# Performance work log

Measured on AMD Instinct MI355X. Metric: run time of the kernel, lower is better.

## Reference

```python
import jax, jax.numpy as jnp
import numpy as np

D = 1024
M = 256
BATCH = 2048


def setup_inputs() -> dict:
    key = jax.random.key(0)
    kx, kw, kp = jax.random.split(key, 3)
    x = jax.random.uniform(kx, (BATCH, D), dtype=jnp.float32)
    W = jax.random.normal(kw, (M,), dtype=jnp.float32)
    P = jax.random.normal(kp, (M, D), dtype=jnp.float32)
    return {"x": x, "W": W, "P": P}


def reference(x, W, P):
    # log mixture weights: log softmax over m
    logw = jax.nn.log_softmax(W, axis=-1)              # [m]
    p = jax.nn.sigmoid(P)                              # [m, d]
    # broadcast Bernoulli likelihood: [batch, m, d]
    lik = x[:, None, :] * p[None, :, :] + (1.0 - x[:, None, :]) * (1.0 - p[None, :, :])
    # per-component log-likelihood summed over features, plus log weight
    comp_ll = jnp.sum(jnp.log(lik), axis=-1) + logw[None, :]   # [batch, m]
    # mixture log-likelihood via logsumexp over components
    return jax.scipy.special.logsumexp(comp_ll, axis=-1)       # [batch]
```

## Files before the change

### kernel.cpp

```cpp
#include <hip/hip_runtime.h>

#define BATCH 2048
#define MM    256
#define DD    1024

#define BB 128
#define BM 64
#define DC 64
#define SD (DD / DC)
#define NBT (BATCH / BB)
#define XS_TILE (DC * BB)
#define RS_TILE (DC * BM)

#define LOG2E 1.4426950408889634f
#define LN2   0.6931471805599453f

typedef float v2f __attribute__((ext_vector_type(2)));

__device__ __forceinline__ float fr_mant(float x) {
    return __builtin_amdgcn_frexp_mantf(x);
}
__device__ __forceinline__ int fr_exp(float x) {
    return __builtin_amdgcn_frexp_expf(x);
}

__device__ __forceinline__ unsigned short f2bf(float f) {
    unsigned u = __float_as_uint(f);
    u += 0x7FFFu + ((u >> 16) & 1u);
    return (unsigned short)(u >> 16);
}
__device__ __forceinline__ float bf2f(unsigned short u) {
    return __uint_as_float((unsigned)u << 16);
}

__device__ __forceinline__ void gl_lds16(const float* g, float* l) {
    __builtin_amdgcn_global_load_lds(
        (const __attribute__((address_space(1))) unsigned int*)g,
        (__attribute__((address_space(3))) unsigned int*)l, 16, 0, 0);
}

__global__ __launch_bounds__(256) void precomp_kernel(
        const float* __restrict__ P, const float* __restrict__ Wv,
        float* __restrict__ rbuf, float* __restrict__ cst) {
    const int m = blockIdx.x;
    const int t = threadIdx.x;
    const int lane = t & 63, wid = t >> 6;

    float4 z = ((const float4*)(P + (size_t)m * DD))[t];
    float e0 = __expf(z.x), e1 = __expf(z.y), e2 = __expf(z.z), e3 = __expf(z.w);
    ((float4*)(rbuf + (size_t)m * DD))[t] =
        make_float4(e0 - 1.f, e1 - 1.f, e2 - 1.f, e3 - 1.f);
    float part = -(__log2f(1.f + e0) + __log2f(1.f + e1) +
                   __log2f(1.f + e2) + __log2f(1.f + e3));

    __shared__ float smA[4], smB[4];

    #pragma unroll
    for (int o = 32; o; o >>= 1) part += __shfl_xor(part, o);
    if (lane == 0) smA[wid] = part;

    float w = Wv[t];
    float mx = w;
    #pragma unroll
    for (int o = 32; o; o >>= 1) mx = fmaxf(mx, __shfl_xor(mx, o));
    if (lane == 0) smB[wid] = mx;
    __syncthreads();

    float rowc = smA[0] + smA[1] + smA[2] + smA[3];
    float gmx  = fmaxf(fmaxf(smB[0], smB[1]), fmaxf(smB[2], smB[3]));

    float se = __expf(w - gmx);
    #pragma unroll
    for (int o = 32; o; o >>= 1) se += __shfl_xor(se, o);
    __syncthreads();
    if (lane == 0) smA[wid] = se;
    __syncthreads();

    if (t == 0) {
        float sum = smA[0] + smA[1] + smA[2] + smA[3];
        cst[m] = rowc + (Wv[m] - gmx) * LOG2E - __log2f(sum);
    }
}

__global__ __launch_bounds__(256) void swz_kernel(
        const float* __restrict__ x, const float* __restrict__ rbuf,
        float* __restrict__ xs, float* __restrict__ rs) {
    __shared__ float t[128 * 65];
    const int tid = threadIdx.x;
    const int bx = blockIdx.x, by = blockIdx.y;

    const float* src;
    float* dst;
    int rows;
    if (bx < NBT) {
        rows = BB;
        src = x + (size_t)bx * BB * DD + by * DC;
        dst = xs + ((size_t)bx * SD + by) * XS_TILE;
    } else {
        rows = BM;
        src = rbuf + (size_t)(bx - NBT) * BM * DD + by * DC;
        dst = rs + ((size_t)(bx - NBT) * SD + by) * RS_TILE;
    }

    const int nf4 = rows * (DC / 4);
    for (int k = 0; k < nf4 / 256; ++k) {
        int idx4 = tid + 256 * k;
        int row = idx4 >> 4;
        int c4  = idx4 & 15;
        float4 v = *(const float4*)(src + (size_t)row * DD + c4 * 4);
        t[row * 65 + c4 * 4 + 0] = v.x;
        t[row * 65 + c4 * 4 + 1] = v.y;
        t[row * 65 + c4 * 4 + 2] = v.z;
        t[row * 65 + c4 * 4 + 3] = v.w;
    }
    __syncthreads();
    const int r4 = rows >> 2;
    for (int k = 0; k < nf4 / 256; ++k) {
        int o4 = tid + 256 * k;
        int kc  = o4 / r4;
        int br4 = o4 - kc * r4;
        float4 w;
        w.x = t[(br4 * 4 + 0) * 65 + kc];
        w.y = t[(br4 * 4 + 1) * 65 + kc];
        w.z = t[(br4 * 4 + 2) * 65 + kc];
        w.w = t[(br4 * 4 + 3) * 65 + kc];
        ((float4*)dst)[o4] = w;
    }
}

__global__ __launch_bounds__(256, 3) void main_kernel(
        const float* __restrict__ xs, const float* __restrict__ rs,
        unsigned short* __restrict__ pbuf) {
    __shared__ __align__(16) float lx[XS_TILE];
    __shared__ __align__(16) float lr[RS_TILE];

    const int tid  = threadIdx.x;
    const int lane = tid & 63;
    const int wv   = tid >> 6;
    const int tx = tid & 15;
    const int ty = tid >> 4;
    const int m_id = blockIdx.x;
    const int b_id = blockIdx.y;
    const int d_id = blockIdx.z;

    const float* xg = xs + ((size_t)b_id * SD + d_id) * XS_TILE;
    const float* rg = rs + ((size_t)m_id * SD + d_id) * RS_TILE;

    #pragma unroll
    for (int k = 0; k < 8; ++k) {
        const int off = (wv * 8 + k) * 256;
        gl_lds16(xg + off + lane * 4, lx + off);
    }
    #pragma unroll
    for (int k = 0; k < 4; ++k) {
        const int off = (wv * 4 + k) * 256;
        gl_lds16(rg + off + lane * 4, lr + off);
    }

    const v2f one2 = {1.0f, 1.0f};
    v2f prod[4][4];
    int acce[8][4];
    #pragma unroll
    for (int i2 = 0; i2 < 4; ++i2)
        #pragma unroll
        for (int j = 0; j < 4; ++j) prod[i2][j] = one2;
    #pragma unroll
    for (int i = 0; i < 8; ++i)
        #pragma unroll
        for (int j = 0; j < 4; ++j) acce[i][j] = 0;

    __syncthreads();

    const float4* xa = (const float4*)(lx + 8 * ty);
    const float4* rb = (const float4*)(lr + 4 * tx);

    #pragma unroll
    for (int g = 0; g < 8; ++g) {
        #pragma unroll
        for (int s = 0; s < 8; ++s) {
            const int kc = g * 8 + s;
            float4 x0 = xa[kc * 32];
            float4 x1 = xa[kc * 32 + 1];
            float4 rv = rb[kc * 16];
            v2f xp2[4] = {{x0.x, x0.y}, {x0.z, x0.w},
                          {x1.x, x1.y}, {x1.z, x1.w}};
            float rf[4] = {rv.x, rv.y, rv.z, rv.w};
            #pragma unroll
            for (int j = 0; j < 4; ++j) {
                v2f rr = {rf[j], rf[j]};
                #pragma unroll
                for (int i2 = 0; i2 < 4; ++i2) {
                    v2f tt = __builtin_elementwise_fma(xp2[i2], rr, one2);
                    prod[i2][j] = prod[i2][j] * tt;
                }
            }
        }
        #pragma unroll
        for (int i2 = 0; i2 < 4; ++i2)
            #pragma unroll
            for (int j = 0; j < 4; ++j) {
                v2f p = prod[i2][j];
                acce[2 * i2 + 0][j] += fr_exp(p.x);
                acce[2 * i2 + 1][j] += fr_exp(p.y);
                p.x = fr_mant(p.x);
                p.y = fr_mant(p.y);
                prod[i2][j] = p;
            }
    }

    unsigned short* pb = pbuf + ((size_t)d_id * BATCH + (size_t)b_id * BB) * MM
                              + (size_t)m_id * BM;
    #pragma unroll
    for (int i2 = 0; i2 < 4; ++i2)
        #pragma unroll
        for (int h = 0; h < 2; ++h) {
            const int i = 2 * i2 + h;
            float f0 = (float)acce[i][0] + __log2f(h ? prod[i2][0].y : prod[i2][0].x);
            float f1 = (float)acce[i][1] + __log2f(h ? prod[i2][1].y : prod[i2][1].x);
            float f2 = (float)acce[i][2] + __log2f(h ? prod[i2][2].y : prod[i2][2].x);
            float f3 = (float)acce[i][3] + __log2f(h ? prod[i2][3].y : prod[i2][3].x);
            ushort4 w;
            w.x = f2bf(f0); w.y = f2bf(f1); w.z = f2bf(f2); w.w = f2bf(f3);
            *(ushort4*)&pb[(size_t)(8 * ty + i) * MM + 4 * tx] = w;
        }
}

__global__ __launch_bounds__(256) void finalize_kernel(
        const unsigned short* __restrict__ pbuf, const float* __restrict__ cst,
        float* __restrict__ out) {
    const int lane = threadIdx.x & 63;
    const int w = threadIdx.x >> 6;
    const int b = blockIdx.x * 4 + w;

    float4 v = ((const float4*)cst)[lane];
    const ushort4* pb = (const ushort4*)pbuf + (size_t)b * (MM / 4) + lane;
    #pragma unroll
    for (int s = 0; s < SD; ++s) {
        ushort4 t = pb[(size_t)s * BATCH * (MM / 4)];
        v.x += bf2f(t.x); v.y += bf2f(t.y); v.z += bf2f(t.z); v.w += bf2f(t.w);
    }

    float mx = fmaxf(fmaxf(v.x, v.y), fmaxf(v.z, v.w));
    #pragma unroll
    for (int o = 32; o; o >>= 1) mx = fmaxf(mx, __shfl_xor(mx, o));

    float s = exp2f(v.x - mx) + exp2f(v.y - mx) + exp2f(v.z - mx) + exp2f(v.w - mx);
    #pragma unroll
    for (int o = 32; o; o >>= 1) s += __shfl_xor(s, o);

    if (lane == 0) out[b] = LN2 * (mx + __log2f(s));
}

extern "C" void kernel_launch(void* const* d_in, const int* in_sizes, int n_in,
                              void* d_out, int out_size, void* d_ws, size_t ws_size,
                              hipStream_t stream) {
    const float* x  = (const float*)d_in[0];
    const float* Wv = (const float*)d_in[1];
    const float* P  = (const float*)d_in[2];

    float* ws   = (float*)d_ws;
    float* xs   = ws;
    float* rs   = xs + (size_t)NBT * SD * XS_TILE;
    float* rbuf = rs + (size_t)(MM / BM) * SD * RS_TILE;
    float* cst  = rbuf + (size_t)MM * DD;
    unsigned short* pbuf = (unsigned short*)(cst + MM);

    precomp_kernel<<<MM, 256, 0, stream>>>(P, Wv, rbuf, cst);
    dim3 gS(NBT + MM / BM, SD);
    swz_kernel<<<gS, 256, 0, stream>>>(x, rbuf, xs, rs);
    dim3 gB(MM / BM, NBT, SD);
    main_kernel<<<gB, 256, 0, stream>>>(xs, rs, pbuf);
    finalize_kernel<<<BATCH / 4, 256, 0, stream>>>(pbuf, cst, (float*)d_out);
}
```

Measured before the change: 111.4 us.

## Merge precompute and swizzle kernels; read x tiles directly from global memory

Fuses the P precompute and the x/r swizzle into one prep kernel that writes the r tile layout directly with scattered stores, which removes the rbuf round trip and one launch. The main kernel no longer stages the x tile in LDS and instead loads x values straight from global/L1 in its inner loop. This shrinks LDS use, so the occupancy hint goes from 3 to 4 blocks. The cost is repeated uncoalesced-ish global loads for x inside the hot loop and strided scalar stores for r.

```diff
diff --git a/kernel.cpp b/kernel.cpp
--- a/kernel.cpp
+++ b/kernel.cpp
@@ -7,8 +7,9 @@
 #define BB 128
 #define BM 64
 #define DC 64
-#define SD (DD / DC)
+#define SD  (DD / DC)
 #define NBT (BATCH / BB)
+#define NMT (MM / BM)
 #define XS_TILE (DC * BB)
 #define RS_TILE (DC * BM)
 
@@ -39,27 +40,70 @@
         (__attribute__((address_space(3))) unsigned int*)l, 16, 0, 0);
 }
 
-__global__ __launch_bounds__(256) void precomp_kernel(
-        const float* __restrict__ P, const float* __restrict__ Wv,
-        float* __restrict__ rbuf, float* __restrict__ cst) {
+__global__ __launch_bounds__(256) void prep_kernel(
+        const float* __restrict__ x, const float* __restrict__ P,
+        const float* __restrict__ Wv, float* __restrict__ xs,
+        float* __restrict__ rs, float* __restrict__ cst) {
+    __shared__ float sh[128 * 65];
+    const int tid = threadIdx.x;
+
+    if (blockIdx.x >= MM) {
+        const int idx = blockIdx.x - MM;
+        const int bx = idx >> 4, by = idx & 15;
+        const float* src = x + (size_t)bx * BB * DD + by * DC;
+        float* dst = xs + ((size_t)bx * SD + by) * XS_TILE;
+
+        #pragma unroll
+        for (int k = 0; k < 8; ++k) {
+            int i4 = tid + 256 * k;
+            int row = i4 >> 4, c4 = i4 & 15;
+            float4 v = *(const float4*)(src + (size_t)row * DD + c4 * 4);
+            sh[row * 65 + c4 * 4 + 0] = v.x;
+            sh[row * 65 + c4 * 4 + 1] = v.y;
+            sh[row * 65 + c4 * 4 + 2] = v.z;
+            sh[row * 65 + c4 * 4 + 3] = v.w;
+        }
+        __syncthreads();
+        #pragma unroll
+        for (int k = 0; k < 8; ++k) {
+            int o4 = tid + 256 * k;
+            int kc = o4 >> 5;
+            int b4 = o4 & 31;
+            float4 w;
+            w.x = sh[(b4 * 4 + 0) * 65 + kc];
+            w.y = sh[(b4 * 4 + 1) * 65 + kc];
+            w.z = sh[(b4 * 4 + 2) * 65 + kc];
+            w.w = sh[(b4 * 4 + 3) * 65 + kc];
+            ((float4*)dst)[o4] = w;
+        }
+        return;
+    }
+
     const int m = blockIdx.x;
-    const int t = threadIdx.x;
-    const int lane = t & 63, wid = t >> 6;
-
-    float4 z = ((const float4*)(P + (size_t)m * DD))[t];
+    const int lane = tid & 63, wid = tid >> 6;
+    float* smA = sh;
+    float* smB = sh + 4;
+
+    float4 z = ((const float4*)(P + (size_t)m * DD))[tid];
     float e0 = __expf(z.x), e1 = __expf(z.y), e2 = __expf(z.z), e3 = __expf(z.w);
-    ((float4*)(rbuf + (size_t)m * DD))[t] =
-        make_float4(e0 - 1.f, e1 - 1.f, e2 - 1.f, e3 - 1.f);
+
+    {
+        const int d_id = tid >> 4;
+        const int kc0  = (4 * tid) & 63;
+        float* rt = rs + ((size_t)(m >> 6) * SD + d_id) * RS_TILE + (m & 63);
+        rt[(size_t)(kc0 + 0) * BM] = e0 - 1.f;
+        rt[(size_t)(kc0 + 1) * BM] = e1 - 1.f;
+        rt[(size_t)(kc0 + 2) * BM] = e2 - 1.f;
+        rt[(size_t)(kc0 + 3) * BM] = e3 - 1.f;
+    }
+
     float part = -(__log2f(1.f + e0) + __log2f(1.f + e1) +
                    __log2f(1.f + e2) + __log2f(1.f + e3));
-
-    __shared__ float smA[4], smB[4];
-
     #pragma unroll
     for (int o = 32; o; o >>= 1) part += __shfl_xor(part, o);
     if (lane == 0) smA[wid] = part;
 
-    float w = Wv[t];
+    float w = Wv[tid];
     float mx = w;
     #pragma unroll
     for (int o = 32; o; o >>= 1) mx = fmaxf(mx, __shfl_xor(mx, o));
@@ -76,62 +120,15 @@
     if (lane == 0) smA[wid] = se;
     __syncthreads();
 
-    if (t == 0) {
+    if (tid == 0) {
         float sum = smA[0] + smA[1] + smA[2] + smA[3];
         cst[m] = rowc + (Wv[m] - gmx) * LOG2E - __log2f(sum);
     }
 }
 
-__global__ __launch_bounds__(256) void swz_kernel(
-        const float* __restrict__ x, const float* __restrict__ rbuf,
-        float* __restrict__ xs, float* __restrict__ rs) {
-    __shared__ float t[128 * 65];
-    const int tid = threadIdx.x;
-    const int bx = blockIdx.x, by = blockIdx.y;
-
-    const float* src;
-    float* dst;
-    int rows;
-    if (bx < NBT) {
-        rows = BB;
-        src = x + (size_t)bx * BB * DD + by * DC;
-        dst = xs + ((size_t)bx * SD + by) * XS_TILE;
-    } else {
-        rows = BM;
-        src = rbuf + (size_t)(bx - NBT) * BM * DD + by * DC;
-        dst = rs + ((size_t)(bx - NBT) * SD + by) * RS_TILE;
-    }
-
-    const int nf4 = rows * (DC / 4);
-    for (int k = 0; k < nf4 / 256; ++k) {
-        int idx4 = tid + 256 * k;
-        int row = idx4 >> 4;
-        int c4  = idx4 & 15;
-        float4 v = *(const float4*)(src + (size_t)row * DD + c4 * 4);
-        t[row * 65 + c4 * 4 + 0] = v.x;
-        t[row * 65 + c4 * 4 + 1] = v.y;
-        t[row * 65 + c4 * 4 + 2] = v.z;
-        t[row * 65 + c4 * 4 + 3] = v.w;
-    }
-    __syncthreads();
-    const int r4 = rows >> 2;
-    for (int k = 0; k < nf4 / 256; ++k) {
-        int o4 = tid + 256 * k;
-        int kc  = o4 / r4;
-        int br4 = o4 - kc * r4;
-        float4 w;
-        w.x = t[(br4 * 4 + 0) * 65 + kc];
-        w.y = t[(br4 * 4 + 1) * 65 + kc];
-        w.z = t[(br4 * 4 + 2) * 65 + kc];
-        w.w = t[(br4 * 4 + 3) * 65 + kc];
-        ((float4*)dst)[o4] = w;
-    }
-}
-
-__global__ __launch_bounds__(256, 3) void main_kernel(
+__global__ __launch_bounds__(256, 4) void main_kernel(
         const float* __restrict__ xs, const float* __restrict__ rs,
         unsigned short* __restrict__ pbuf) {
-    __shared__ __align__(16) float lx[XS_TILE];
     __shared__ __align__(16) float lr[RS_TILE];
 
     const int tid  = threadIdx.x;
@@ -143,20 +140,15 @@
     const int b_id = blockIdx.y;
     const int d_id = blockIdx.z;
 
-    const float* xg = xs + ((size_t)b_id * SD + d_id) * XS_TILE;
     const float* rg = rs + ((size_t)m_id * SD + d_id) * RS_TILE;
-
-    #pragma unroll
-    for (int k = 0; k < 8; ++k) {
-        const int off = (wv * 8 + k) * 256;
-        gl_lds16(xg + off + lane * 4, lx + off);
-    }
     #pragma unroll
     for (int k = 0; k < 4; ++k) {
         const int off = (wv * 4 + k) * 256;
         gl_lds16(rg + off + lane * 4, lr + off);
     }
 
+    const float* xg = xs + ((size_t)b_id * SD + d_id) * XS_TILE + 8 * ty;
+
     const v2f one2 = {1.0f, 1.0f};
     v2f prod[4][4];
     int acce[8][4];
@@ -171,17 +163,16 @@
 
     __syncthreads();
 
-    const float4* xa = (const float4*)(lx + 8 * ty);
-    const float4* rb = (const float4*)(lr + 4 * tx);
+    const float* rp = lr + 4 * tx;
 
     #pragma unroll
     for (int g = 0; g < 8; ++g) {
         #pragma unroll
         for (int s = 0; s < 8; ++s) {
             const int kc = g * 8 + s;
-            float4 x0 = xa[kc * 32];
-            float4 x1 = xa[kc * 32 + 1];
-            float4 rv = rb[kc * 16];
+            float4 x0 = *(const float4*)(xg + kc * BB);
+            float4 x1 = *(const float4*)(xg + kc * BB + 4);
+            float4 rv = *(const float4*)(rp + kc * BM);
             v2f xp2[4] = {{x0.x, x0.y}, {x0.z, x0.w},
                           {x1.x, x1.y}, {x1.z, x1.w}};
             float rf[4] = {rv.x, rv.y, rv.z, rv.w};
@@ -258,17 +249,14 @@
     const float* Wv = (const float*)d_in[1];
     const float* P  = (const float*)d_in[2];
 
-    float* ws   = (float*)d_ws;
-    float* xs   = ws;
-    float* rs   = xs + (size_t)NBT * SD * XS_TILE;
-    float* rbuf = rs + (size_t)(MM / BM) * SD * RS_TILE;
-    float* cst  = rbuf + (size_t)MM * DD;
+    float* ws  = (float*)d_ws;
+    float* xs  = ws;
+    float* rs  = xs + (size_t)NBT * SD * XS_TILE;
+    float* cst = rs + (size_t)NMT * SD * RS_TILE;
     unsigned short* pbuf = (unsigned short*)(cst + MM);
 
-    precomp_kernel<<<MM, 256, 0, stream>>>(P, Wv, rbuf, cst);
-    dim3 gS(NBT + MM / BM, SD);
-    swz_kernel<<<gS, 256, 0, stream>>>(x, rbuf, xs, rs);
-    dim3 gB(MM / BM, NBT, SD);
+    prep_kernel<<<MM + NBT * SD, 256, 0, stream>>>(x, P, Wv, xs, rs, cst);
+    dim3 gB(NMT, NBT, SD);
     main_kernel<<<gB, 256, 0, stream>>>(xs, rs, pbuf);
     finalize_kernel<<<BATCH / 4, 256, 0, stream>>>(pbuf, cst, (float*)d_out);
 }
```

Result: slower. 123.4 us (+10.8%).

## Fuse transpose into main kernel via padded LDS and halve the D chunk

Applied to the files above, without the earlier changes.

Drops the separate swizzle kernel and its pre-transposed xs/rs buffers. The main kernel now reads x and rbuf directly from global memory and transposes them on the fly into padded shared-memory tiles. The D chunk is halved to 32 and the occupancy hint raised to 6 blocks per CU, which shrinks shared memory per block. In exchange, the number of D chunks doubles, so the bf16 partial-sum buffer and the finalize reduction work double. The scalar transposed LDS stores may also add store cost.

```diff
diff --git a/kernel.cpp b/kernel.cpp
--- a/kernel.cpp
+++ b/kernel.cpp
@@ -6,11 +6,12 @@
 
 #define BB 128
 #define BM 64
-#define DC 64
-#define SD (DD / DC)
+#define DC 32
+#define SD  (DD / DC)
 #define NBT (BATCH / BB)
-#define XS_TILE (DC * BB)
-#define RS_TILE (DC * BM)
+#define NMT (MM / BM)
+#define LXS (BB + 4)
+#define LRS (BM + 4)
 
 #define LOG2E 1.4426950408889634f
 #define LN2   0.6931471805599453f
@@ -31,12 +32,6 @@
 }
 __device__ __forceinline__ float bf2f(unsigned short u) {
     return __uint_as_float((unsigned)u << 16);
-}
-
-__device__ __forceinline__ void gl_lds16(const float* g, float* l) {
-    __builtin_amdgcn_global_load_lds(
-        (const __attribute__((address_space(1))) unsigned int*)g,
-        (__attribute__((address_space(3))) unsigned int*)l, 16, 0, 0);
 }
 
 __global__ __launch_bounds__(256) void precomp_kernel(
@@ -82,79 +77,43 @@
     }
 }
 
-__global__ __launch_bounds__(256) void swz_kernel(
+__global__ __launch_bounds__(256, 6) void main_kernel(
         const float* __restrict__ x, const float* __restrict__ rbuf,
-        float* __restrict__ xs, float* __restrict__ rs) {
-    __shared__ float t[128 * 65];
+        unsigned short* __restrict__ pbuf) {
+    __shared__ __align__(16) float lx[DC * LXS];
+    __shared__ __align__(16) float lr[DC * LRS];
+
     const int tid = threadIdx.x;
-    const int bx = blockIdx.x, by = blockIdx.y;
-
-    const float* src;
-    float* dst;
-    int rows;
-    if (bx < NBT) {
-        rows = BB;
-        src = x + (size_t)bx * BB * DD + by * DC;
-        dst = xs + ((size_t)bx * SD + by) * XS_TILE;
-    } else {
-        rows = BM;
-        src = rbuf + (size_t)(bx - NBT) * BM * DD + by * DC;
-        dst = rs + ((size_t)(bx - NBT) * SD + by) * RS_TILE;
-    }
-
-    const int nf4 = rows * (DC / 4);
-    for (int k = 0; k < nf4 / 256; ++k) {
-        int idx4 = tid + 256 * k;
-        int row = idx4 >> 4;
-        int c4  = idx4 & 15;
-        float4 v = *(const float4*)(src + (size_t)row * DD + c4 * 4);
-        t[row * 65 + c4 * 4 + 0] = v.x;
-        t[row * 65 + c4 * 4 + 1] = v.y;
-        t[row * 65 + c4 * 4 + 2] = v.z;
-        t[row * 65 + c4 * 4 + 3] = v.w;
-    }
-    __syncthreads();
-    const int r4 = rows >> 2;
-    for (int k = 0; k < nf4 / 256; ++k) {
-        int o4 = tid + 256 * k;
-        int kc  = o4 / r4;
-        int br4 = o4 - kc * r4;
-        float4 w;
-        w.x = t[(br4 * 4 + 0) * 65 + kc];
-        w.y = t[(br4 * 4 + 1) * 65 + kc];
-        w.z = t[(br4 * 4 + 2) * 65 + kc];
-        w.w = t[(br4 * 4 + 3) * 65 + kc];
-        ((float4*)dst)[o4] = w;
-    }
-}
-
-__global__ __launch_bounds__(256, 3) void main_kernel(
-        const float* __restrict__ xs, const float* __restrict__ rs,
-        unsigned short* __restrict__ pbuf) {
-    __shared__ __align__(16) float lx[XS_TILE];
-    __shared__ __align__(16) float lr[RS_TILE];
-
-    const int tid  = threadIdx.x;
-    const int lane = tid & 63;
-    const int wv   = tid >> 6;
     const int tx = tid & 15;
     const int ty = tid >> 4;
     const int m_id = blockIdx.x;
     const int b_id = blockIdx.y;
     const int d_id = blockIdx.z;
-
-    const float* xg = xs + ((size_t)b_id * SD + d_id) * XS_TILE;
-    const float* rg = rs + ((size_t)m_id * SD + d_id) * RS_TILE;
-
-    #pragma unroll
-    for (int k = 0; k < 8; ++k) {
-        const int off = (wv * 8 + k) * 256;
-        gl_lds16(xg + off + lane * 4, lx + off);
-    }
-    #pragma unroll
-    for (int k = 0; k < 4; ++k) {
-        const int off = (wv * 4 + k) * 256;
-        gl_lds16(rg + off + lane * 4, lr + off);
+    const int m0 = m_id * BM;
+    const int b0 = b_id * BB;
+    const int d0 = d_id * DC;
+
+    #pragma unroll
+    for (int l = 0; l < 4; ++l) {
+        int i4 = tid + 256 * l;
+        int row = i4 >> 3;
+        int seg = i4 & 7;
+        float4 v = *(const float4*)(x + (size_t)(b0 + row) * DD + d0 + seg * 4);
+        lx[(seg * 4 + 0) * LXS + row] = v.x;
+        lx[(seg * 4 + 1) * LXS + row] = v.y;
+        lx[(seg * 4 + 2) * LXS + row] = v.z;
+        lx[(seg * 4 + 3) * LXS + row] = v.w;
+    }
+    #pragma unroll
+    for (int l = 0; l < 2; ++l) {
+        int i4 = tid + 256 * l;
+        int row = i4 >> 3;
+        int seg = i4 & 7;
+        float4 v = *(const float4*)(rbuf + (size_t)(m0 + row) * DD + d0 + seg * 4);
+        lr[(seg * 4 + 0) * LRS + row] = v.x;
+        lr[(seg * 4 + 1) * LRS + row] = v.y;
+        lr[(seg * 4 + 2) * LRS + row] = v.z;
+        lr[(seg * 4 + 3) * LRS + row] = v.w;
     }
 
     const v2f one2 = {1.0f, 1.0f};
@@ -175,13 +134,13 @@
     const float4* rb = (const float4*)(lr + 4 * tx);
 
     #pragma unroll
-    for (int g = 0; g < 8; ++g) {
+    for (int g = 0; g < 4; ++g) {
         #pragma unroll
         for (int s = 0; s < 8; ++s) {
             const int kc = g * 8 + s;
-            float4 x0 = xa[kc * 32];
-            float4 x1 = xa[kc * 32 + 1];
-            float4 rv = rb[kc * 16];
+            float4 x0 = xa[kc * 33];
+            float4 x1 = xa[kc * 33 + 1];
+            float4 rv = rb[kc * 17];
             v2f xp2[4] = {{x0.x, x0.y}, {x0.z, x0.w},
                           {x1.x, x1.y}, {x1.z, x1.w}};
             float rf[4] = {rv.x, rv.y, rv.z, rv.w};
@@ -208,8 +167,7 @@
             }
     }
 
-    unsigned short* pb = pbuf + ((size_t)d_id * BATCH + (size_t)b_id * BB) * MM
-                              + (size_t)m_id * BM;
+    unsigned short* pb = pbuf + ((size_t)d_id * BATCH + (size_t)b0) * MM + m0;
     #pragma unroll
     for (int i2 = 0; i2 < 4; ++i2)
         #pragma unroll
@@ -259,16 +217,12 @@
     const float* P  = (const float*)d_in[2];
 
     float* ws   = (float*)d_ws;
-    float* xs   = ws;
-    float* rs   = xs + (size_t)NBT * SD * XS_TILE;
-    float* rbuf = rs + (size_t)(MM / BM) * SD * RS_TILE;
+    float* rbuf = ws;
     float* cst  = rbuf + (size_t)MM * DD;
     unsigned short* pbuf = (unsigned short*)(cst + MM);
 
     precomp_kernel<<<MM, 256, 0, stream>>>(P, Wv, rbuf, cst);
-    dim3 gS(NBT + MM / BM, SD);
-    swz_kernel<<<gS, 256, 0, stream>>>(x, rbuf, xs, rs);
-    dim3 gB(MM / BM, NBT, SD);
-    main_kernel<<<gB, 256, 0, stream>>>(xs, rs, pbuf);
+    dim3 gB(NMT, NBT, SD);
+    main_kernel<<<gB, 256, 0, stream>>>(x, rbuf, pbuf);
     finalize_kernel<<<BATCH / 4, 256, 0, stream>>>(pbuf, cst, (float*)d_out);
 }
```

After: 150.6 us. +35.2%, slower.
